# Performance work log

Hardware: AMD Instinct MI355X
Metric: run time of the kernel (lower is better)

Reference implementation:

```python
import jax, jax.numpy as jnp
import numpy as np

D_MODEL = 1024
N_HEADS = 16
D_HEAD = D_MODEL // N_HEADS


def setup_inputs() -> dict:
    key = jax.random.key(0)
    ks = jax.random.split(key, 9)
    B, S = 2, 2048
    s = 0.02
    return {
        "x": jax.random.normal(ks[0], (B, S, D_MODEL), dtype=jnp.float32),
        "Wq": jax.random.normal(ks[1], (D_MODEL, D_MODEL), dtype=jnp.float32) * s,
        "bq": jnp.zeros((D_MODEL,), dtype=jnp.float32),
        "Wk": jax.random.normal(ks[2], (D_MODEL, D_MODEL), dtype=jnp.float32) * s,
        "bk": jnp.zeros((D_MODEL,), dtype=jnp.float32),
        "Wv": jax.random.normal(ks[3], (D_MODEL, D_MODEL), dtype=jnp.float32) * s,
        "bv": jnp.zeros((D_MODEL,), dtype=jnp.float32),
        "Wo": jax.random.normal(ks[4], (D_MODEL, D_MODEL), dtype=jnp.float32) * s,
        "bo": jnp.zeros((D_MODEL,), dtype=jnp.float32),
    }


def reference(x, Wq, bq, Wk, bk, Wv, bv, Wo, bo):
    B, S, _ = x.shape
    # projections -> [B, H, S, Dh]
    def split_heads(t):
        return t.reshape(B, S, N_HEADS, D_HEAD).transpose(0, 2, 1, 3)
    Q = split_heads(x @ Wq + bq)
    K = split_heads(x @ Wk + bk)
    V = split_heads(x @ Wv + bv)
    scores = jnp.einsum('bhqd,bhkd->bhqk', Q, K)  # [B,H,S,S]
    mask = jnp.tril(jnp.ones((S, S), dtype=bool))
    # NB: original masks BEFORE scaling (mask fill -1e9 then /sqrt(d_head))
    scores = jnp.where(mask[None, None], scores, jnp.float32(-1e9))
    scores = scores / jnp.sqrt(jnp.float32(D_HEAD))
    attn = jax.nn.softmax(scores, axis=-1)
    ctx = jnp.einsum('bhqk,bhkd->bhqd', attn, V)
    ctx = ctx.transpose(0, 2, 1, 3).reshape(B, S, D_MODEL)
    return ctx @ Wo + bo
```

## Files before the change

### kernel.cpp

```cpp
#include <hip/hip_runtime.h>

typedef __bf16 bf16;
typedef __bf16 bf16x8 __attribute__((ext_vector_type(8)));
typedef __bf16 bf16x4 __attribute__((ext_vector_type(4)));
typedef float  f32x4  __attribute__((ext_vector_type(4)));

#define D_MODEL 1024
#define S_LEN   2048
#define NHEAD   16
#define DHEAD   64
#define BATCH   2
#define MROWS   (BATCH * S_LEN)

#define QSCALE 0.18033688011112042f

__device__ __forceinline__ void gld_lds16(const void* g, void* lds_base) {
    __builtin_amdgcn_global_load_lds(
        (const __attribute__((address_space(1))) void*)g,
        (__attribute__((address_space(3))) void*)lds_base, 16, 0, 0);
}

__global__ void prep_kernel(const float* __restrict__ x,
                            const float* __restrict__ W0, const float* __restrict__ W1,
                            const float* __restrict__ W2, const float* __restrict__ W3,
                            bf16* __restrict__ xb, bf16* __restrict__ Wt) {
    int tx = threadIdx.x, ty = threadIdx.y;
    if (blockIdx.z == 4) {
        int tid = ty * 32 + tx;
        size_t base = ((size_t)blockIdx.y * 32 + blockIdx.x) * 4096;
#pragma unroll
        for (int j = 0; j < 4; j++) {
            size_t i = base + (size_t)(j * 256 + tid) * 4;
            f32x4 v = *(const f32x4*)(x + i);
            bf16x4 o;
            o[0] = (bf16)v[0]; o[1] = (bf16)v[1]; o[2] = (bf16)v[2]; o[3] = (bf16)v[3];
            *(bf16x4*)(xb + i) = o;
        }
        return;
    }
    __shared__ float tile[32][33];
    const float* W = (blockIdx.z == 0) ? W0 : (blockIdx.z == 1) ? W1
                   : (blockIdx.z == 2) ? W2 : W3;
    int n0 = blockIdx.x * 32, k0 = blockIdx.y * 32;
#pragma unroll
    for (int j = 0; j < 4; j++)
        tile[ty + 8 * j][tx] = W[(size_t)(k0 + ty + 8 * j) * D_MODEL + n0 + tx];
    __syncthreads();
    bf16* out = Wt + (size_t)blockIdx.z * D_MODEL * D_MODEL;
#pragma unroll
    for (int j = 0; j < 4; j++)
        out[(size_t)(n0 + ty + 8 * j) * D_MODEL + k0 + tx] = (bf16)tile[tx][ty + 8 * j];
}

template <int MODE>
__global__ __launch_bounds__(256, 2) void gemm_kernel(
    const bf16* __restrict__ A, const bf16* __restrict__ Bt,
    const float* __restrict__ b0, const float* __restrict__ b1, const float* __restrict__ b2,
    bf16* __restrict__ Qo, bf16* __restrict__ Ko, bf16* __restrict__ Vto,
    float* __restrict__ Co) {
    __shared__ bf16 sA[128 * 32];
    __shared__ bf16 sB[128 * 32];
    const int t = threadIdx.x;
    const int wave = t >> 6, lane = t & 63;
    const int wm = wave >> 1, wn = wave & 1;
    const int quad = lane >> 4, m16 = lane & 15;
    const int row0 = blockIdx.y * 128, col0 = blockIdx.x * 128;
    const int K = D_MODEL;

    f32x4 acc[4][4];
#pragma unroll
    for (int i = 0; i < 4; i++)
#pragma unroll
        for (int j = 0; j < 4; j++) acc[i][j] = (f32x4){0.f, 0.f, 0.f, 0.f};

    for (int kk = 0; kk < K; kk += 32) {
#pragma unroll
        for (int i = 0; i < 2; i++) {
            int cb = i * 256 + wave * 64;
            int c  = cb + lane;
            int r  = c >> 2, kg = c & 3;
            gld_lds16(A  + (size_t)(row0 + r) * K + kk + kg * 8, (char*)sA + cb * 16);
            gld_lds16(Bt + (size_t)(col0 + r) * K + kk + kg * 8, (char*)sB + cb * 16);
        }
        __syncthreads();
        bf16x8 af[4], bfr[4];
#pragma unroll
        for (int mi = 0; mi < 4; mi++)
            af[mi] = *(const bf16x8*)&sA[(wm * 64 + mi * 16 + m16) * 32 + quad * 8];
#pragma unroll
        for (int ni = 0; ni < 4; ni++)
            bfr[ni] = *(const bf16x8*)&sB[(wn * 64 + ni * 16 + m16) * 32 + quad * 8];
#pragma unroll
        for (int mi = 0; mi < 4; mi++)
#pragma unroll
            for (int ni = 0; ni < 4; ni++)
                acc[mi][ni] = __builtin_amdgcn_mfma_f32_16x16x32_bf16(
                    af[mi], bfr[ni], acc[mi][ni], 0, 0, 0);
        __syncthreads();
    }

    if (MODE == 1) {
#pragma unroll
        for (int mi = 0; mi < 4; mi++) {
            int r0 = row0 + wm * 64 + mi * 16 + quad * 4;
#pragma unroll
            for (int ni = 0; ni < 4; ni++) {
                int col = col0 + wn * 64 + ni * 16 + m16;
                float bias = b0[col];
#pragma unroll
                for (int r = 0; r < 4; r++)
                    Co[(size_t)(r0 + r) * D_MODEL + col] = acc[mi][ni][r] + bias;
            }
        }
    } else {
        int sel = col0 >> 10;
        const float* bias_arr = (sel == 0) ? b0 : (sel == 1) ? b1 : b2;
#pragma unroll
        for (int mi = 0; mi < 4; mi++) {
            int s0g = row0 + wm * 64 + mi * 16 + quad * 4;
            int b = s0g >> 11, ss0 = s0g & 2047;
#pragma unroll
            for (int ni = 0; ni < 4; ni++) {
                int col = col0 + wn * 64 + ni * 16 + m16;
                int cn = col & 1023;
                int h = cn >> 6, d = cn & 63;
                float bias = bias_arr[cn];
                if (sel < 2) {
                    bf16* dst = (sel == 0) ? Qo : Ko;
                    float scl = (sel == 0) ? QSCALE : 1.0f;
                    size_t base = (((size_t)b * NHEAD + h) * S_LEN);
#pragma unroll
                    for (int r = 0; r < 4; r++)
                        dst[(base + ss0 + r) * DHEAD + d] = (bf16)((acc[mi][ni][r] + bias) * scl);
                } else {
                    bf16x4 pk;
#pragma unroll
                    for (int r = 0; r < 4; r++) pk[r] = (bf16)(acc[mi][ni][r] + bias);
                    *(bf16x4*)(Vto + (((size_t)b * NHEAD + h) * DHEAD + d) * S_LEN + ss0) = pk;
                }
            }
        }
    }
}

__global__ __launch_bounds__(256, 2) void attn_kernel(
    const bf16* __restrict__ Q, const bf16* __restrict__ K,
    const bf16* __restrict__ Vt, bf16* __restrict__ ctx) {
    __shared__ bf16 Kt_s[3][64 * 64];
    __shared__ bf16 Vt_s[3][64 * 64];
    __shared__ bf16 P_s[4][2][16 * 72];

    const int t = threadIdx.x, wave = t >> 6, lane = t & 63;
    const int quad = lane >> 4, m16 = lane & 15;
    const int bh = blockIdx.y, p = blockIdx.x;
    const int tT[2] = {p, 31 - p};
    const int nt = 32 - p;
    const size_t base = (size_t)bh * S_LEN * DHEAD;

    bf16x8 aq[2][2];
#pragma unroll
    for (int it = 0; it < 2; it++)
#pragma unroll
        for (int kst = 0; kst < 2; kst++)
            aq[it][kst] = *(const bf16x8*)(Q + base
                + (size_t)(tT[it] * 64 + wave * 16 + m16) * DHEAD + kst * 32 + quad * 8);

    f32x4 o[2][4];
#pragma unroll
    for (int it = 0; it < 2; it++)
#pragma unroll
        for (int di = 0; di < 4; di++) o[it][di] = (f32x4){0.f, 0.f, 0.f, 0.f};
    float l_acc[2] = {0.f, 0.f};

    auto stage = [&](int j, int buf) {
#pragma unroll
        for (int i = 0; i < 2; i++) {
            int cb = i * 256 + wave * 64;
            int c  = cb + lane;
            int pos = c >> 3, g = c & 7;
            int gk = g ^ (pos & 7);
            gld_lds16(K  + base + (size_t)(j * 64 + pos) * DHEAD + gk * 8,
                      (char*)&Kt_s[buf][0] + cb * 16);
            gld_lds16(Vt + base + (size_t)pos * S_LEN + j * 64 + gk * 8,
                      (char*)&Vt_s[buf][0] + cb * 16);
        }
    };

    stage(0, 0);
    if (nt > 1) stage(1, 1);

    for (int j = 0; j < nt; ++j) {
        if (j + 1 < nt) asm volatile("s_waitcnt vmcnt(4)\n\ts_barrier" ::: "memory");
        else            asm volatile("s_waitcnt vmcnt(0)\n\ts_barrier" ::: "memory");
        if (j + 2 < nt) stage(j + 2, (j + 2) % 3);

        const int cur = j % 3;
        const bool aAct = (j <= tT[0]);
        const int kt0 = j * 64;

        auto computeTile = [&](bool both) {
            int itlo = both ? 0 : 1;
            f32x4 sc[2][4];
#pragma unroll
            for (int it = 0; it < 2; it++)
#pragma unroll
                for (int ni = 0; ni < 4; ni++) sc[it][ni] = (f32x4){0.f, 0.f, 0.f, 0.f};
#pragma unroll
            for (int ni = 0; ni < 4; ni++) {
                int pos = ni * 16 + m16;
#pragma unroll
                for (int kst = 0; kst < 2; kst++) {
                    int gg = (kst * 4 + quad) ^ (pos & 7);
                    bf16x8 kf = *(const bf16x8*)&Kt_s[cur][pos * 64 + gg * 8];
                    sc[1][ni] = __builtin_amdgcn_mfma_f32_16x16x32_bf16(
                        kf, aq[1][kst], sc[1][ni], 0, 0, 0);
                    if (both)
                        sc[0][ni] = __builtin_amdgcn_mfma_f32_16x16x32_bf16(
                            kf, aq[0][kst], sc[0][ni], 0, 0, 0);
                }
            }
#pragma unroll
            for (int it = 0; it < 2; it++) {
                if (it < itlo) continue;
                if (j == tT[it]) {
                    int qg = tT[it] * 64 + wave * 16 + m16;
#pragma unroll
                    for (int ni = 0; ni < 4; ni++)
#pragma unroll
                        for (int r = 0; r < 4; r++) {
                            int kp = kt0 + ni * 16 + quad * 4 + r;
                            if (kp > qg) sc[it][ni][r] = -1e9f;
                        }
                }
            }
#pragma unroll
            for (int it = 0; it < 2; it++) {
                if (it < itlo) continue;
                bf16* Pw = &P_s[wave][it][0];
                float ls = 0.f;
#pragma unroll
                for (int ni = 0; ni < 4; ni++) {
                    bf16x4 pk;
#pragma unroll
                    for (int r = 0; r < 4; r++) {
                        float pe = __builtin_amdgcn_exp2f(sc[it][ni][r]);
                        ls += pe;
                        pk[r] = (bf16)pe;
                    }
                    *(bf16x4*)&Pw[m16 * 72 + ni * 16 + quad * 4] = pk;
                }
                l_acc[it] += ls;
            }
#pragma unroll
            for (int kst = 0; kst < 2; kst++) {
                bf16x8 ap[2];
#pragma unroll
                for (int it = 0; it < 2; it++)
                    if (it >= itlo)
                        ap[it] = *(const bf16x8*)&P_s[wave][it][m16 * 72 + kst * 32 + quad * 8];
#pragma unroll
                for (int di = 0; di < 4; di++) {
                    int d = di * 16 + m16;
                    int gg = (kst * 4 + quad) ^ (d & 7);
                    bf16x8 vf = *(const bf16x8*)&Vt_s[cur][d * 64 + gg * 8];
                    o[1][di] = __builtin_amdgcn_mfma_f32_16x16x32_bf16(
                        vf, ap[1], o[1][di], 0, 0, 0);
                    if (both)
                        o[0][di] = __builtin_amdgcn_mfma_f32_16x16x32_bf16(
                            vf, ap[0], o[0][di], 0, 0, 0);
                }
            }
        };
        if (aAct) computeTile(true);
        else      computeTile(false);
    }

    int b = bh >> 4, h = bh & 15;
#pragma unroll
    for (int it = 0; it < 2; it++) {
        float l = l_acc[it];
        l += __shfl_xor(l, 16);
        l += __shfl_xor(l, 32);
        float rl = 1.0f / l;
        int s = tT[it] * 64 + wave * 16 + m16;
#pragma unroll
        for (int di = 0; di < 4; di++) {
            bf16x4 pk;
#pragma unroll
            for (int r = 0; r < 4; r++) pk[r] = (bf16)(o[it][di][r] * rl);
            *(bf16x4*)(ctx + ((size_t)b * S_LEN + s) * D_MODEL
                       + h * DHEAD + di * 16 + quad * 4) = pk;
        }
    }
}

extern "C" void kernel_launch(void* const* d_in, const int* in_sizes, int n_in,
                              void* d_out, int out_size, void* d_ws, size_t ws_size,
                              hipStream_t stream) {
    const float* x  = (const float*)d_in[0];
    const float* Wq = (const float*)d_in[1];
    const float* bq = (const float*)d_in[2];
    const float* Wk = (const float*)d_in[3];
    const float* bk = (const float*)d_in[4];
    const float* Wv = (const float*)d_in[5];
    const float* bv = (const float*)d_in[6];
    const float* Wo = (const float*)d_in[7];
    const float* bo = (const float*)d_in[8];
    float* out = (float*)d_out;

    char* ws = (char*)d_ws;
    const size_t MB = 1u << 20;
    bf16* xb  = (bf16*)(ws + 0);
    bf16* Wt  = (bf16*)(ws + 8  * MB);
    bf16* Qb  = (bf16*)(ws + 16 * MB);
    bf16* Kb  = (bf16*)(ws + 24 * MB);
    bf16* Vtb = (bf16*)(ws + 32 * MB);
    bf16* ctx = (bf16*)(ws + 0);

    prep_kernel<<<dim3(32, 32, 5), dim3(32, 8), 0, stream>>>(x, Wq, Wk, Wv, Wo, xb, Wt);
    gemm_kernel<0><<<dim3(24, 32), 256, 0, stream>>>(xb, Wt, bq, bk, bv,
                                                     Qb, Kb, Vtb, nullptr);
    attn_kernel<<<dim3(16, 32), 256, 0, stream>>>(Qb, Kb, Vtb, ctx);
    gemm_kernel<1><<<dim3(8, 32), 256, 0, stream>>>(ctx, Wt + 3 * 1024 * 1024,
                                                    bo, nullptr, nullptr,
                                                    nullptr, nullptr, nullptr, out);
}
```

Baseline: 190.2 us.

## Keep softmax probabilities in registers via permlane32 swap instead of LDS

Result: no change. 193.1 us (+1.5%).

```diff
diff --git a/kernel.cpp b/kernel.cpp
--- a/kernel.cpp
+++ b/kernel.cpp
@@ -148,7 +148,6 @@
     const bf16* __restrict__ Vt, bf16* __restrict__ ctx) {
     __shared__ bf16 Kt_s[3][64 * 64];
     __shared__ bf16 Vt_s[3][64 * 64];
-    __shared__ bf16 P_s[4][2][16 * 72];
 
     const int t = threadIdx.x, wave = t >> 6, lane = t & 63;
     const int quad = lane >> 4, m16 = lane & 15;
@@ -205,6 +204,7 @@
             for (int it = 0; it < 2; it++)
 #pragma unroll
                 for (int ni = 0; ni < 4; ni++) sc[it][ni] = (f32x4){0.f, 0.f, 0.f, 0.f};
+            __builtin_amdgcn_s_setprio(1);
 #pragma unroll
             for (int ni = 0; ni < 4; ni++) {
                 int pos = ni * 16 + m16;
@@ -219,6 +219,7 @@
                             kf, aq[0][kst], sc[0][ni], 0, 0, 0);
                 }
             }
+            __builtin_amdgcn_s_setprio(0);
 #pragma unroll
             for (int it = 0; it < 2; it++) {
                 if (it < itlo) continue;
@@ -233,42 +234,58 @@
                         }
                 }
             }
+            unsigned int pd[2][4][2];
 #pragma unroll
             for (int it = 0; it < 2; it++) {
                 if (it < itlo) continue;
-                bf16* Pw = &P_s[wave][it][0];
-                float ls = 0.f;
+                float ls0 = 0.f, ls1 = 0.f;
 #pragma unroll
                 for (int ni = 0; ni < 4; ni++) {
-                    bf16x4 pk;
-#pragma unroll
-                    for (int r = 0; r < 4; r++) {
-                        float pe = __builtin_amdgcn_exp2f(sc[it][ni][r]);
-                        ls += pe;
-                        pk[r] = (bf16)pe;
-                    }
-                    *(bf16x4*)&Pw[m16 * 72 + ni * 16 + quad * 4] = pk;
-                }
-                l_acc[it] += ls;
+                    float p0 = __builtin_amdgcn_exp2f(sc[it][ni][0]);
+                    float p1 = __builtin_amdgcn_exp2f(sc[it][ni][1]);
+                    float p2 = __builtin_amdgcn_exp2f(sc[it][ni][2]);
+                    float p3 = __builtin_amdgcn_exp2f(sc[it][ni][3]);
+                    union { bf16x4 h; unsigned int u[2]; } cv;
+                    cv.h[0] = (bf16)p0; cv.h[1] = (bf16)p1;
+                    cv.h[2] = (bf16)p2; cv.h[3] = (bf16)p3;
+                    pd[it][ni][0] = cv.u[0];
+                    pd[it][ni][1] = cv.u[1];
+                    ls0 += p0 + p1;
+                    ls1 += p2 + p3;
+                }
+                l_acc[it] += ls0 + ls1;
             }
 #pragma unroll
             for (int kst = 0; kst < 2; kst++) {
                 bf16x8 ap[2];
 #pragma unroll
-                for (int it = 0; it < 2; it++)
-                    if (it >= itlo)
-                        ap[it] = *(const bf16x8*)&P_s[wave][it][m16 * 72 + kst * 32 + quad * 8];
+                for (int it = 0; it < 2; it++) {
+                    if (it < itlo) continue;
+                    unsigned int a1 = pd[it][2 * kst][0], b1 = pd[it][2 * kst + 1][0];
+                    unsigned int a2 = pd[it][2 * kst][1], b2 = pd[it][2 * kst + 1][1];
+                    asm("v_permlane32_swap_b32 %0, %1" : "+v"(a1), "+v"(b1));
+                    asm("v_permlane32_swap_b32 %0, %1" : "+v"(a2), "+v"(b2));
+                    union { unsigned int u[4]; bf16x8 v; } pk;
+                    pk.u[0] = a1; pk.u[1] = a2; pk.u[2] = b1; pk.u[3] = b2;
+                    ap[it] = pk.v;
+                }
+                const int bq0 = kst * 8 + ((quad >> 1) << 2) + (quad & 1);
+                const int ob  = (bq0 & 1) << 3;
+                __builtin_amdgcn_s_setprio(1);
 #pragma unroll
                 for (int di = 0; di < 4; di++) {
                     int d = di * 16 + m16;
-                    int gg = (kst * 4 + quad) ^ (d & 7);
-                    bf16x8 vf = *(const bf16x8*)&Vt_s[cur][d * 64 + gg * 8];
+                    const char* rowp = (const char*)&Vt_s[cur][0] + d * 128;
+                    union { bf16x4 h[2]; bf16x8 v; } vv;
+                    vv.h[0] = *(const bf16x4*)(rowp + ((((bq0 >> 1) + 0) ^ (d & 7)) << 4) + ob);
+                    vv.h[1] = *(const bf16x4*)(rowp + ((((bq0 >> 1) + 1) ^ (d & 7)) << 4) + ob);
                     o[1][di] = __builtin_amdgcn_mfma_f32_16x16x32_bf16(
-                        vf, ap[1], o[1][di], 0, 0, 0);
+                        vv.v, ap[1], o[1][di], 0, 0, 0);
                     if (both)
                         o[0][di] = __builtin_amdgcn_mfma_f32_16x16x32_bf16(
-                            vf, ap[0], o[0][di], 0, 0, 0);
-                }
+                            vv.v, ap[0], o[0][di], 0, 0, 0);
+                }
+                __builtin_amdgcn_s_setprio(0);
             }
         };
         if (aAct) computeTile(true);
```
